# Kernel tuning notes

Measured on AMD Instinct MI355X. Metric: run time of the kernel, lower is better.

## Reference

```python
import jax, jax.numpy as jnp
import numpy as np

HIDDEN = 2048
REDUCTION = 4
DOWN = HIDDEN // REDUCTION  # 512
E = 16
K = 2
B, S = 4, 2048


def setup_inputs() -> dict:
    key = jax.random.key(0)
    k1, k2, k3, k4 = jax.random.split(key, 4)
    x = jax.random.normal(k1, (B, S, HIDDEN), dtype=jnp.float32)
    gate_w = jax.random.normal(k2, (E, HIDDEN), dtype=jnp.float32) * 0.02
    # xavier_uniform over (E, DOWN, HIDDEN): bound = sqrt(6/(DOWN+HIDDEN))
    bound = float(np.sqrt(6.0 / (DOWN + HIDDEN)))
    down_w = jax.random.uniform(k3, (E, DOWN, HIDDEN), dtype=jnp.float32,
                                minval=-bound, maxval=bound)
    down_b = jnp.zeros((E, DOWN), dtype=jnp.float32)
    ub = float(np.sqrt(1.0 / DOWN))
    up_w = jax.random.uniform(k4, (HIDDEN, DOWN), dtype=jnp.float32,
                              minval=-ub, maxval=ub)
    up_b = jnp.zeros((HIDDEN,), dtype=jnp.float32)
    return {"x": x, "gate_w": gate_w, "down_w": down_w, "down_b": down_b,
            "up_w": up_w, "up_b": up_b}


def reference(x, gate_w, down_w, down_b, up_w, up_b):
    Bb, Ss, D = x.shape
    N = Bb * Ss
    xf = x.reshape(N, D)
    # TopKGate: logits -> top-k -> softmax over the k logits -> scatter to full [N,E]
    logits = xf @ gate_w.T                       # [N, E]
    topv, topi = jax.lax.top_k(logits, K)        # [N, K]
    probs = jax.nn.softmax(topv, axis=-1)        # [N, K]
    gw = jnp.zeros_like(logits).at[jnp.arange(N)[:, None], topi].set(probs)  # [N, E]
    # Dense-equivalent of gather + per-token bmm + scatter-add combine:
    # final[n] = sum_e gw[n,e] * (down_w[e] @ x[n] + down_b[e])
    expert_out = jnp.einsum('nd,eod->neo', xf, down_w) + down_b[None]  # [N, E, DOWN]
    combined = jnp.einsum('ne,neo->no', gw, expert_out)                # [N, DOWN]
    h = jax.nn.gelu(combined, approximate=True)  # gelu_new (tanh approx)
    h = h.reshape(Bb, Ss, DOWN)
    out = h @ up_w.T + up_b                      # [B, S, HIDDEN]
    # load balancing loss: E * sum(sum(gw,0)/N * mean(gw,0)) * alpha
    loss = E * jnp.sum(jnp.sum(gw, axis=0) / N * jnp.mean(gw, axis=0)) * 0.1
    return out, loss
```

## Files before the change

kernel.cpp:

```cpp
#include <hip/hip_runtime.h>
#include <hip/hip_bf16.h>
#include <math.h>

#define NTOK   8192
#define HID    2048
#define DWN    512
#define NEXP   16
#define PADSLOT 18432

#define OFF_COMBINED 0
#define OFF_XB       16777216
#define OFF_DWB      50331648
#define OFF_UWB      83886080
#define OFF_H        85983232
#define OFF_TOK      94371840
#define OFF_PROB     94445568
#define OFF_EIDX     94519296
#define OFF_PVAL     94584832
#define OFF_COUNTS   94650368
#define OFF_BASE     94650432
#define OFF_CURSOR   94650560
#define OFF_COLSUM   94650624
#define WS_NEEDED    94650688

typedef __attribute__((ext_vector_type(8))) __bf16 bf16x8;
typedef __attribute__((ext_vector_type(4))) float f32x4;

#define ASYNC16(gsrc, ldst) \
  __builtin_amdgcn_global_load_lds((const __attribute__((address_space(1))) unsigned int*)(gsrc), \
                                   (__attribute__((address_space(3))) unsigned int*)(ldst), 16, 0, 0)

__device__ inline unsigned short f2bf(float f) {
  unsigned int u = __float_as_uint(f);
  unsigned int r = (u + 0x7FFFu + ((u >> 16) & 1u)) >> 16;
  return (unsigned short)r;
}

__global__ __launch_bounds__(256) void cast8_kernel(const float* __restrict__ src,
                                                    unsigned short* __restrict__ dst)
{
  size_t i = ((size_t)blockIdx.x * 256 + threadIdx.x) * 8;
  float4 a = *(const float4*)(src + i);
  float4 b = *(const float4*)(src + i + 4);
  unsigned short o[8];
  o[0]=f2bf(a.x); o[1]=f2bf(a.y); o[2]=f2bf(a.z); o[3]=f2bf(a.w);
  o[4]=f2bf(b.x); o[5]=f2bf(b.y); o[6]=f2bf(b.z); o[7]=f2bf(b.w);
  *(uint4*)(dst + i) = *(const uint4*)o;
}

__global__ __launch_bounds__(256) void gate_kernel(
    const float* __restrict__ x, const float* __restrict__ gw,
    int2* __restrict__ eidx, float2* __restrict__ pvals)
{
  int lane = threadIdx.x & 63;
  int wave = threadIdx.x >> 6;
  int n = blockIdx.x * 4 + wave;
  const float* xr  = x + (size_t)n * HID;
  const float* gwp = gw + lane;

  double a0=0,a1=0,a2=0,a3=0,a4=0,a5=0,a6=0,a7=0;
  double a8=0,a9=0,a10=0,a11=0,a12=0,a13=0,a14=0,a15=0;

  for (int d0 = 0; d0 < HID; d0 += 64) {
    double xd = (double)xr[d0 + lane];
    const float* g = gwp + d0;
    a0  = fma(xd, (double)g[ 0*HID], a0);
    a1  = fma(xd, (double)g[ 1*HID], a1);
    a2  = fma(xd, (double)g[ 2*HID], a2);
    a3  = fma(xd, (double)g[ 3*HID], a3);
    a4  = fma(xd, (double)g[ 4*HID], a4);
    a5  = fma(xd, (double)g[ 5*HID], a5);
    a6  = fma(xd, (double)g[ 6*HID], a6);
    a7  = fma(xd, (double)g[ 7*HID], a7);
    a8  = fma(xd, (double)g[ 8*HID], a8);
    a9  = fma(xd, (double)g[ 9*HID], a9);
    a10 = fma(xd, (double)g[10*HID], a10);
    a11 = fma(xd, (double)g[11*HID], a11);
    a12 = fma(xd, (double)g[12*HID], a12);
    a13 = fma(xd, (double)g[13*HID], a13);
    a14 = fma(xd, (double)g[14*HID], a14);
    a15 = fma(xd, (double)g[15*HID], a15);
  }

#define RED(v) { v += __shfl_xor(v,32,64); v += __shfl_xor(v,16,64); v += __shfl_xor(v,8,64); \
                 v += __shfl_xor(v,4,64);  v += __shfl_xor(v,2,64);  v += __shfl_xor(v,1,64); }
  RED(a0) RED(a1) RED(a2) RED(a3) RED(a4) RED(a5) RED(a6) RED(a7)
  RED(a8) RED(a9) RED(a10) RED(a11) RED(a12) RED(a13) RED(a14) RED(a15)
#undef RED

  if (lane == 0) {
    double v0 = -1e300, v1 = -1e300;
    int i0 = 0, i1 = 0;
#define TOP(v,E) { if ((v) > v0) { v1 = v0; i1 = i0; v0 = (v); i0 = (E); } \
                   else if ((v) > v1) { v1 = (v); i1 = (E); } }
    TOP(a0,0) TOP(a1,1) TOP(a2,2) TOP(a3,3) TOP(a4,4) TOP(a5,5) TOP(a6,6) TOP(a7,7)
    TOP(a8,8) TOP(a9,9) TOP(a10,10) TOP(a11,11) TOP(a12,12) TOP(a13,13) TOP(a14,14) TOP(a15,15)
#undef TOP
    double ex = exp(v1 - v0);
    double denom = 1.0 + ex;
    eidx[n]  = make_int2(i0, i1);
    pvals[n] = make_float2((float)(1.0 / denom), (float)(ex / denom));
  }
}

__global__ __launch_bounds__(256) void hist_kernel(
    const int2* __restrict__ eidx, const float2* __restrict__ pvals,
    int* __restrict__ counts, float* __restrict__ colsum)
{
  __shared__ int   cbin[NEXP];
  __shared__ float lbin[NEXP];
  if (threadIdx.x < NEXP) { cbin[threadIdx.x] = 0; lbin[threadIdx.x] = 0.f; }
  __syncthreads();
  int n = blockIdx.x * 256 + threadIdx.x;
  int2 e = eidx[n];
  float2 p = pvals[n];
  atomicAdd(&cbin[e.x], 1);  atomicAdd(&lbin[e.x], p.x);
  atomicAdd(&cbin[e.y], 1);  atomicAdd(&lbin[e.y], p.y);
  __syncthreads();
  if (threadIdx.x < NEXP) {
    atomicAdd(&counts[threadIdx.x], cbin[threadIdx.x]);
    atomicAdd(&colsum[threadIdx.x], lbin[threadIdx.x]);
  }
}

__global__ void scan_loss_kernel(const int* __restrict__ counts, int* __restrict__ base,
                                 const float* __restrict__ colsum, float* __restrict__ loss_out)
{
  if (threadIdx.x == 0 && blockIdx.x == 0) {
    int acc = 0;
    for (int e = 0; e < NEXP; e++) { base[e] = acc; acc += (counts[e] + 127) & ~127; }
    base[NEXP] = acc;
    double s = 0.0;
    for (int e = 0; e < NEXP; e++) { double c = (double)colsum[e]; s += c * c; }
    loss_out[0] = (float)(1.6 * s / ((double)NTOK * (double)NTOK));
  }
}

__global__ __launch_bounds__(256) void scatter_kernel(
    const int2* __restrict__ eidx, const float2* __restrict__ pvals,
    const int* __restrict__ base, int* __restrict__ cursor,
    int* __restrict__ tok, float* __restrict__ prob)
{
  int n = blockIdx.x * 256 + threadIdx.x;
  int lane = threadIdx.x & 63;
  int2 e = eidx[n];
  float2 p = pvals[n];
  int   myE[2] = {e.x, e.y};
  float myP[2] = {p.x, p.y};
#pragma unroll
  for (int s = 0; s < 2; s++) {
    int eq = myE[s];
#pragma unroll
    for (int q = 0; q < NEXP; q++) {
      unsigned long long m = __ballot(eq == q);
      if (eq == q) {
        int cnt = __popcll(m);
        int pre = __popcll(m & ((1ull << lane) - 1ull));
        int b = 0;
        if (pre == 0) b = atomicAdd(&cursor[q], cnt);
        int leader = __ffsll((long long)m) - 1;
        b = __shfl(b, leader, 64);
        int pos = base[q] + b + pre;
        tok[pos] = n; prob[pos] = myP[s];
      }
    }
  }
}

__global__ __launch_bounds__(256) void down_mfma_kernel(
    const unsigned short* __restrict__ xb, const unsigned short* __restrict__ dwb,
    const float* __restrict__ db,
    const int* __restrict__ base, const int* __restrict__ tok, const float* __restrict__ prob,
    float* __restrict__ combined)
{
  __shared__ unsigned short As[128 * 64];
  __shared__ unsigned short Bs[128 * 64];
  __shared__ int   tks[128];
  __shared__ float prs[128];

  int slot0 = blockIdx.x * 128;
  if (slot0 >= base[NEXP]) return;
  int e = 0;
#pragma unroll
  for (int q = 1; q < NEXP; q++) if (base[q] <= slot0) e = q;
  int out0 = blockIdx.y * 128;

  int tid = threadIdx.x;
  if (tid < 128) { tks[tid] = tok[slot0 + tid]; prs[tid] = prob[slot0 + tid]; }

  const int l = tid & 63, w = tid >> 6;
  const int wm = w & 1, wn = w >> 1;
  const int lm = l & 15, quad = l >> 4;

  const unsigned short* agp[4];
  const unsigned short* bgp[4];
#pragma unroll
  for (int i = 0; i < 4; i++) {
    int c = (w * 4 + i) * 64 + l;
    int r = c >> 3, kc = c & 7;
    int t = tok[slot0 + r];
    agp[i] = xb + (size_t)(t < 0 ? 0 : t) * HID + kc * 8;
    bgp[i] = dwb + ((size_t)e * DWN + out0 + r) * HID + kc * 8;
  }

  f32x4 acc[4][4] = {};

  for (int k0 = 0; k0 < HID; k0 += 64) {
    __syncthreads();
#pragma unroll
    for (int i = 0; i < 4; i++) {
      ASYNC16(agp[i] + k0, &As[(w * 4 + i) * 64 * 8]);
      ASYNC16(bgp[i] + k0, &Bs[(w * 4 + i) * 64 * 8]);
    }
    __syncthreads();
#pragma unroll
    for (int kk = 0; kk < 64; kk += 32) {
      bf16x8 af[4], bfr[4];
#pragma unroll
      for (int mi = 0; mi < 4; mi++)
        af[mi] = *(const bf16x8*)&As[(wm * 64 + mi * 16 + lm) * 64 + kk + quad * 8];
#pragma unroll
      for (int ni = 0; ni < 4; ni++)
        bfr[ni] = *(const bf16x8*)&Bs[(wn * 64 + ni * 16 + lm) * 64 + kk + quad * 8];
#pragma unroll
      for (int mi = 0; mi < 4; mi++)
#pragma unroll
        for (int ni = 0; ni < 4; ni++)
          acc[mi][ni] = __builtin_amdgcn_mfma_f32_16x16x32_bf16(af[mi], bfr[ni], acc[mi][ni], 0, 0, 0);
    }
  }

  float dbv[4];
#pragma unroll
  for (int ni = 0; ni < 4; ni++)
    dbv[ni] = db[e * DWN + out0 + wn * 64 + ni * 16 + lm];
#pragma unroll
  for (int mi = 0; mi < 4; mi++) {
#pragma unroll
    for (int reg = 0; reg < 4; reg++) {
      int m = wm * 64 + mi * 16 + quad * 4 + reg;
      int t = tks[m];
      if (t < 0) continue;
      float p = prs[m];
      float* crow = combined + (size_t)t * DWN;
#pragma unroll
      for (int ni = 0; ni < 4; ni++) {
        int gc = out0 + wn * 64 + ni * 16 + lm;
        atomicAdd(&crow[gc], p * (acc[mi][ni][reg] + dbv[ni]));
      }
    }
  }
}

__global__ __launch_bounds__(256) void gelu_cast_kernel(const float* __restrict__ c,
                                                        unsigned short* __restrict__ h)
{
  size_t i = ((size_t)blockIdx.x * 256 + threadIdx.x) * 8;
  float4 a = *(const float4*)(c + i);
  float4 b = *(const float4*)(c + i + 4);
  float f[8] = {a.x, a.y, a.z, a.w, b.x, b.y, b.z, b.w};
  unsigned short o[8];
#pragma unroll
  for (int j = 0; j < 8; j++) {
    float xx = f[j];
    float inner = 0.7978845608028654f * (xx + 0.044715f * xx * xx * xx);
    o[j] = f2bf(0.5f * xx * (1.0f + tanhf(inner)));
  }
  *(uint4*)(h + i) = *(const uint4*)o;
}

__global__ __launch_bounds__(256) void up_mfma_kernel(
    const unsigned short* __restrict__ h, const unsigned short* __restrict__ uwb,
    const float* __restrict__ ub, float* __restrict__ out)
{
  __shared__ unsigned short As[128 * 64];
  __shared__ unsigned short Bs[128 * 64];

  int row0 = blockIdx.x * 128;
  int col0 = blockIdx.y * 128;
  int tid = threadIdx.x;
  const int l = tid & 63, w = tid >> 6;
  const int wm = w & 1, wn = w >> 1;
  const int lm = l & 15, quad = l >> 4;

  const unsigned short* agp[4];
  const unsigned short* bgp[4];
#pragma unroll
  for (int i = 0; i < 4; i++) {
    int c = (w * 4 + i) * 64 + l;
    int r = c >> 3, kc = c & 7;
    agp[i] = h   + (size_t)(row0 + r) * DWN + kc * 8;
    bgp[i] = uwb + (size_t)(col0 + r) * DWN + kc * 8;
  }

  f32x4 acc[4][4] = {};

  for (int k0 = 0; k0 < DWN; k0 += 64) {
    __syncthreads();
#pragma unroll
    for (int i = 0; i < 4; i++) {
      ASYNC16(agp[i] + k0, &As[(w * 4 + i) * 64 * 8]);
      ASYNC16(bgp[i] + k0, &Bs[(w * 4 + i) * 64 * 8]);
    }
    __syncthreads();
#pragma unroll
    for (int kk = 0; kk < 64; kk += 32) {
      bf16x8 af[4], bfr[4];
#pragma unroll
      for (int mi = 0; mi < 4; mi++)
        af[mi] = *(const bf16x8*)&As[(wm * 64 + mi * 16 + lm) * 64 + kk + quad * 8];
#pragma unroll
      for (int ni = 0; ni < 4; ni++)
        bfr[ni] = *(const bf16x8*)&Bs[(wn * 64 + ni * 16 + lm) * 64 + kk + quad * 8];
#pragma unroll
      for (int mi = 0; mi < 4; mi++)
#pragma unroll
        for (int ni = 0; ni < 4; ni++)
          acc[mi][ni] = __builtin_amdgcn_mfma_f32_16x16x32_bf16(af[mi], bfr[ni], acc[mi][ni], 0, 0, 0);
    }
  }

  float ubv[4];
#pragma unroll
  for (int ni = 0; ni < 4; ni++)
    ubv[ni] = ub[col0 + wn * 64 + ni * 16 + lm];
#pragma unroll
  for (int mi = 0; mi < 4; mi++) {
#pragma unroll
    for (int reg = 0; reg < 4; reg++) {
      int m = row0 + wm * 64 + mi * 16 + quad * 4 + reg;
      float* orow = out + (size_t)m * HID;
#pragma unroll
      for (int ni = 0; ni < 4; ni++) {
        int gc = col0 + wn * 64 + ni * 16 + lm;
        orow[gc] = acc[mi][ni][reg] + ubv[ni];
      }
    }
  }
}

extern "C" void kernel_launch(void* const* d_in, const int* in_sizes, int n_in,
                              void* d_out, int out_size, void* d_ws, size_t ws_size,
                              hipStream_t stream)
{
  const float* x  = (const float*)d_in[0];
  const float* gw = (const float*)d_in[1];
  const float* dw = (const float*)d_in[2];
  const float* db = (const float*)d_in[3];
  const float* uw = (const float*)d_in[4];
  const float* ub = (const float*)d_in[5];
  float* out = (float*)d_out;

  char* ws = (char*)d_ws;
  float*          combined = (float*)(ws + OFF_COMBINED);
  unsigned short* xb       = (unsigned short*)(ws + OFF_XB);
  unsigned short* dwb      = (unsigned short*)(ws + OFF_DWB);
  unsigned short* uwb      = (unsigned short*)(ws + OFF_UWB);
  unsigned short* h        = (unsigned short*)(ws + OFF_H);
  int*    tok    = (int*)(ws + OFF_TOK);
  float*  prob   = (float*)(ws + OFF_PROB);
  int2*   eidx   = (int2*)(ws + OFF_EIDX);
  float2* pvals  = (float2*)(ws + OFF_PVAL);
  int*    counts = (int*)(ws + OFF_COUNTS);
  int*    base   = (int*)(ws + OFF_BASE);
  int*    cursor = (int*)(ws + OFF_CURSOR);
  float*  colsum = (float*)(ws + OFF_COLSUM);

  hipMemsetAsync(combined, 0, (size_t)NTOK * DWN * sizeof(float), stream);
  hipMemsetAsync(tok, 0xFF, PADSLOT * sizeof(int), stream);
  hipMemsetAsync(counts, 0, WS_NEEDED - OFF_COUNTS, stream);

  cast8_kernel<<<(NTOK * HID) / 8 / 256, 256, 0, stream>>>(x, xb);
  cast8_kernel<<<(NEXP * DWN * HID) / 8 / 256, 256, 0, stream>>>(dw, dwb);
  cast8_kernel<<<(HID * DWN) / 8 / 256, 256, 0, stream>>>(uw, uwb);

  gate_kernel<<<NTOK / 4, 256, 0, stream>>>(x, gw, eidx, pvals);
  hist_kernel<<<NTOK / 256, 256, 0, stream>>>(eidx, pvals, counts, colsum);
  scan_loss_kernel<<<1, 64, 0, stream>>>(counts, base, colsum, out + (size_t)NTOK * HID);
  scatter_kernel<<<NTOK / 256, 256, 0, stream>>>(eidx, pvals, base, cursor, tok, prob);

  dim3 gdown(PADSLOT / 128, DWN / 128);
  down_mfma_kernel<<<gdown, 256, 0, stream>>>(xb, dwb, db, base, tok, prob, combined);

  gelu_cast_kernel<<<(NTOK * DWN) / 8 / 256, 256, 0, stream>>>(combined, h);

  dim3 gup(NTOK / 128, HID / 128);
  up_mfma_kernel<<<gup, 256, 0, stream>>>(h, uwb, ub, out);
}
```

Baseline: 434.4 us.

## Replace atomic scatter-add combine with bf16 slot buffers and fused combine+GELU

```diff
diff --git a/kernel.cpp b/kernel.cpp
--- a/kernel.cpp
+++ b/kernel.cpp
@@ -8,20 +8,23 @@
 #define NEXP   16
 #define PADSLOT 18432
 
-#define OFF_COMBINED 0
-#define OFF_XB       16777216
-#define OFF_DWB      50331648
-#define OFF_UWB      83886080
-#define OFF_H        85983232
-#define OFF_TOK      94371840
-#define OFF_PROB     94445568
-#define OFF_EIDX     94519296
-#define OFF_PVAL     94584832
-#define OFF_COUNTS   94650368
-#define OFF_BASE     94650432
-#define OFF_CURSOR   94650560
-#define OFF_COLSUM   94650624
-#define WS_NEEDED    94650688
+#define OFF_XB       0
+#define OFF_DWB      33554432
+#define OFF_H        33554432
+#define OFF_UWB      67108864
+#define OFF_TOK      69206016
+#define OFF_SPOS     69279744
+#define OFF_EIDX     69345280
+#define OFF_PVAL     69410816
+#define OFF_COUNTS   69476352
+#define OFF_BASE     69476416
+#define OFF_CURSOR   69476544
+#define OFF_COLSUM   69476608
+#define OFF_SEG      69476672
+#define SEGHALF_SHORTS 9437184
+#define SEGHALF_BYTES  18874368
+#define WS_NEED1     (OFF_SEG + 1 * SEGHALF_BYTES)
+#define WS_NEED2     (OFF_SEG + 2 * SEGHALF_BYTES)
 
 typedef __attribute__((ext_vector_type(8))) __bf16 bf16x8;
 typedef __attribute__((ext_vector_type(4))) float f32x4;
@@ -34,6 +37,9 @@
   unsigned int u = __float_as_uint(f);
   unsigned int r = (u + 0x7FFFu + ((u >> 16) & 1u)) >> 16;
   return (unsigned short)r;
+}
+__device__ inline float bf2f(unsigned short s) {
+  return __uint_as_float((unsigned int)s << 16);
 }
 
 __global__ __launch_bounds__(256) void cast8_kernel(const float* __restrict__ src,
@@ -137,16 +143,14 @@
 }
 
 __global__ __launch_bounds__(256) void scatter_kernel(
-    const int2* __restrict__ eidx, const float2* __restrict__ pvals,
-    const int* __restrict__ base, int* __restrict__ cursor,
-    int* __restrict__ tok, float* __restrict__ prob)
+    const int2* __restrict__ eidx, const int* __restrict__ base, int* __restrict__ cursor,
+    int* __restrict__ tok, int2* __restrict__ spos)
 {
   int n = blockIdx.x * 256 + threadIdx.x;
   int lane = threadIdx.x & 63;
   int2 e = eidx[n];
-  float2 p = pvals[n];
-  int   myE[2] = {e.x, e.y};
-  float myP[2] = {p.x, p.y};
+  int myE[2] = {e.x, e.y};
+  int myPos[2];
 #pragma unroll
   for (int s = 0; s < 2; s++) {
     int eq = myE[s];
@@ -161,22 +165,22 @@
         int leader = __ffsll((long long)m) - 1;
         b = __shfl(b, leader, 64);
         int pos = base[q] + b + pre;
-        tok[pos] = n; prob[pos] = myP[s];
+        tok[pos] = n;
+        myPos[s] = pos;
       }
     }
   }
+  spos[n] = make_int2(myPos[0], myPos[1]);
 }
 
 __global__ __launch_bounds__(256) void down_mfma_kernel(
     const unsigned short* __restrict__ xb, const unsigned short* __restrict__ dwb,
-    const float* __restrict__ db,
-    const int* __restrict__ base, const int* __restrict__ tok, const float* __restrict__ prob,
-    float* __restrict__ combined)
-{
-  __shared__ unsigned short As[128 * 64];
-  __shared__ unsigned short Bs[128 * 64];
-  __shared__ int   tks[128];
-  __shared__ float prs[128];
+    const int* __restrict__ base, const int* __restrict__ tok,
+    unsigned short* __restrict__ seg, int kcount)
+{
+  __shared__ unsigned short smem[17408];
+  unsigned short* As = smem;
+  unsigned short* Bs = smem + 8192;
 
   int slot0 = blockIdx.x * 128;
   if (slot0 >= base[NEXP]) return;
@@ -184,10 +188,10 @@
 #pragma unroll
   for (int q = 1; q < NEXP; q++) if (base[q] <= slot0) e = q;
   int out0 = blockIdx.y * 128;
+  int kh   = blockIdx.z;
+  int kbase = kh * kcount * 64;
 
   int tid = threadIdx.x;
-  if (tid < 128) { tks[tid] = tok[slot0 + tid]; prs[tid] = prob[slot0 + tid]; }
-
   const int l = tid & 63, w = tid >> 6;
   const int wm = w & 1, wn = w >> 1;
   const int lm = l & 15, quad = l >> 4;
@@ -196,32 +200,42 @@
   const unsigned short* bgp[4];
 #pragma unroll
   for (int i = 0; i < 4; i++) {
-    int c = (w * 4 + i) * 64 + l;
-    int r = c >> 3, kc = c & 7;
+    int g = w * 4 + i;
+    int r = g * 8 + (l & 7);
+    int kc = l >> 3;
     int t = tok[slot0 + r];
-    agp[i] = xb + (size_t)(t < 0 ? 0 : t) * HID + kc * 8;
-    bgp[i] = dwb + ((size_t)e * DWN + out0 + r) * HID + kc * 8;
+    agp[i] = xb + (size_t)(t < 0 ? 0 : t) * HID + kbase + kc * 8;
+    bgp[i] = dwb + ((size_t)e * DWN + out0 + r) * HID + kbase + kc * 8;
+  }
+
+  int am_off[4], bn_off[4];
+#pragma unroll
+  for (int mi = 0; mi < 4; mi++) {
+    int m = wm * 64 + mi * 16 + lm;
+    am_off[mi] = (m >> 3) * 512 + (m & 7) * 8 + quad * 64;
+    int nn = wn * 64 + mi * 16 + lm;
+    bn_off[mi] = (nn >> 3) * 512 + (nn & 7) * 8 + quad * 64;
   }
 
   f32x4 acc[4][4] = {};
 
-  for (int k0 = 0; k0 < HID; k0 += 64) {
+  for (int it = 0; it < kcount; it++) {
+    int k0 = it * 64;
     __syncthreads();
 #pragma unroll
     for (int i = 0; i < 4; i++) {
-      ASYNC16(agp[i] + k0, &As[(w * 4 + i) * 64 * 8]);
-      ASYNC16(bgp[i] + k0, &Bs[(w * 4 + i) * 64 * 8]);
+      int g = w * 4 + i;
+      ASYNC16(agp[i] + k0, &As[g * 512]);
+      ASYNC16(bgp[i] + k0, &Bs[g * 512]);
     }
     __syncthreads();
 #pragma unroll
-    for (int kk = 0; kk < 64; kk += 32) {
+    for (int kk = 0; kk < 2; kk++) {
       bf16x8 af[4], bfr[4];
 #pragma unroll
-      for (int mi = 0; mi < 4; mi++)
-        af[mi] = *(const bf16x8*)&As[(wm * 64 + mi * 16 + lm) * 64 + kk + quad * 8];
-#pragma unroll
-      for (int ni = 0; ni < 4; ni++)
-        bfr[ni] = *(const bf16x8*)&Bs[(wn * 64 + ni * 16 + lm) * 64 + kk + quad * 8];
+      for (int mi = 0; mi < 4; mi++) af[mi]  = *(const bf16x8*)&As[am_off[mi] + kk * 256];
+#pragma unroll
+      for (int ni = 0; ni < 4; ni++) bfr[ni] = *(const bf16x8*)&Bs[bn_off[ni] + kk * 256];
 #pragma unroll
       for (int mi = 0; mi < 4; mi++)
 #pragma unroll
@@ -230,51 +244,72 @@
     }
   }
 
-  float dbv[4];
-#pragma unroll
-  for (int ni = 0; ni < 4; ni++)
-    dbv[ni] = db[e * DWN + out0 + wn * 64 + ni * 16 + lm];
-#pragma unroll
-  for (int mi = 0; mi < 4; mi++) {
+  __syncthreads();
+#pragma unroll
+  for (int mi = 0; mi < 4; mi++)
 #pragma unroll
     for (int reg = 0; reg < 4; reg++) {
       int m = wm * 64 + mi * 16 + quad * 4 + reg;
-      int t = tks[m];
-      if (t < 0) continue;
-      float p = prs[m];
-      float* crow = combined + (size_t)t * DWN;
 #pragma unroll
       for (int ni = 0; ni < 4; ni++) {
-        int gc = out0 + wn * 64 + ni * 16 + lm;
-        atomicAdd(&crow[gc], p * (acc[mi][ni][reg] + dbv[ni]));
+        int c = wn * 64 + ni * 16 + lm;
+        smem[m * 136 + c] = f2bf(acc[mi][ni][reg]);
       }
     }
-  }
-}
-
-__global__ __launch_bounds__(256) void gelu_cast_kernel(const float* __restrict__ c,
-                                                        unsigned short* __restrict__ h)
-{
-  size_t i = ((size_t)blockIdx.x * 256 + threadIdx.x) * 8;
-  float4 a = *(const float4*)(c + i);
-  float4 b = *(const float4*)(c + i + 4);
-  float f[8] = {a.x, a.y, a.z, a.w, b.x, b.y, b.z, b.w};
+  __syncthreads();
+#pragma unroll
+  for (int it2 = 0; it2 < 8; it2++) {
+    int chunk = it2 * 256 + tid;
+    int row = chunk >> 4, off = (chunk & 15) * 8;
+    uint4 v = *(const uint4*)&smem[row * 136 + off];
+    *(uint4*)&seg[(size_t)kh * SEGHALF_SHORTS + (size_t)(slot0 + row) * 512 + out0 + off] = v;
+  }
+}
+
+__global__ __launch_bounds__(256) void combine_gelu_kernel(
+    const unsigned short* __restrict__ seg, const int2* __restrict__ spos,
+    const float2* __restrict__ pv, const int2* __restrict__ eix,
+    const float* __restrict__ db, unsigned short* __restrict__ h, int ksplit)
+{
+  int n = blockIdx.x * 4 + (threadIdx.x >> 6);
+  int lane = threadIdx.x & 63;
+  int c0 = lane * 8;
+  int2 sp = spos[n];
+  float2 p = pv[n];
+  int2 e = eix[n];
+
+  float d0[8] = {0,0,0,0,0,0,0,0}, d1[8] = {0,0,0,0,0,0,0,0};
+  for (int hh = 0; hh < ksplit; hh++) {
+    uint4 u0 = *(const uint4*)(seg + (size_t)hh * SEGHALF_SHORTS + (size_t)sp.x * 512 + c0);
+    uint4 u1 = *(const uint4*)(seg + (size_t)hh * SEGHALF_SHORTS + (size_t)sp.y * 512 + c0);
+    const unsigned short* s0 = (const unsigned short*)&u0;
+    const unsigned short* s1 = (const unsigned short*)&u1;
+#pragma unroll
+    for (int j = 0; j < 8; j++) { d0[j] += bf2f(s0[j]); d1[j] += bf2f(s1[j]); }
+  }
+  float b0[8], b1[8];
+  *(float4*)&b0[0] = *(const float4*)(db + e.x * DWN + c0);
+  *(float4*)&b0[4] = *(const float4*)(db + e.x * DWN + c0 + 4);
+  *(float4*)&b1[0] = *(const float4*)(db + e.y * DWN + c0);
+  *(float4*)&b1[4] = *(const float4*)(db + e.y * DWN + c0 + 4);
+
   unsigned short o[8];
 #pragma unroll
   for (int j = 0; j < 8; j++) {
-    float xx = f[j];
+    float xx = p.x * (d0[j] + b0[j]) + p.y * (d1[j] + b1[j]);
     float inner = 0.7978845608028654f * (xx + 0.044715f * xx * xx * xx);
     o[j] = f2bf(0.5f * xx * (1.0f + tanhf(inner)));
   }
-  *(uint4*)(h + i) = *(const uint4*)o;
+  *(uint4*)(h + (size_t)n * DWN + c0) = *(const uint4*)o;
 }
 
 __global__ __launch_bounds__(256) void up_mfma_kernel(
     const unsigned short* __restrict__ h, const unsigned short* __restrict__ uwb,
     const float* __restrict__ ub, float* __restrict__ out)
 {
-  __shared__ unsigned short As[128 * 64];
-  __shared__ unsigned short Bs[128 * 64];
+  __shared__ unsigned short smem[16384];
+  unsigned short* As = smem;
+  unsigned short* Bs = smem + 8192;
 
   int row0 = blockIdx.x * 128;
   int col0 = blockIdx.y * 128;
@@ -287,31 +322,40 @@
   const unsigned short* bgp[4];
 #pragma unroll
   for (int i = 0; i < 4; i++) {
-    int c = (w * 4 + i) * 64 + l;
-    int r = c >> 3, kc = c & 7;
+    int g = w * 4 + i;
+    int r = g * 8 + (l & 7);
+    int kc = l >> 3;
     agp[i] = h   + (size_t)(row0 + r) * DWN + kc * 8;
     bgp[i] = uwb + (size_t)(col0 + r) * DWN + kc * 8;
   }
 
+  int am_off[4], bn_off[4];
+#pragma unroll
+  for (int mi = 0; mi < 4; mi++) {
+    int m = wm * 64 + mi * 16 + lm;
+    am_off[mi] = (m >> 3) * 512 + (m & 7) * 8 + quad * 64;
+    int nn = wn * 64 + mi * 16 + lm;
+    bn_off[mi] = (nn >> 3) * 512 + (nn & 7) * 8 + quad * 64;
+  }
+
   f32x4 acc[4][4] = {};
 
   for (int k0 = 0; k0 < DWN; k0 += 64) {
     __syncthreads();
 #pragma unroll
     for (int i = 0; i < 4; i++) {
-      ASYNC16(agp[i] + k0, &As[(w * 4 + i) * 64 * 8]);
-      ASYNC16(bgp[i] + k0, &Bs[(w * 4 + i) * 64 * 8]);
+      int g = w * 4 + i;
+      ASYNC16(agp[i] + k0, &As[g * 512]);
+      ASYNC16(bgp[i] + k0, &Bs[g * 512]);
     }
     __syncthreads();
 #pragma unroll
-    for (int kk = 0; kk < 64; kk += 32) {
+    for (int kk = 0; kk < 2; kk++) {
       bf16x8 af[4], bfr[4];
 #pragma unroll
-      for (int mi = 0; mi < 4; mi++)
-        af[mi] = *(const bf16x8*)&As[(wm * 64 + mi * 16 + lm) * 64 + kk + quad * 8];
-#pragma unroll
-      for (int ni = 0; ni < 4; ni++)
-        bfr[ni] = *(const bf16x8*)&Bs[(wn * 64 + ni * 16 + lm) * 64 + kk + quad * 8];
+      for (int mi = 0; mi < 4; mi++) af[mi]  = *(const bf16x8*)&As[am_off[mi] + kk * 256];
+#pragma unroll
+      for (int ni = 0; ni < 4; ni++) bfr[ni] = *(const bf16x8*)&Bs[bn_off[ni] + kk * 256];
 #pragma unroll
       for (int mi = 0; mi < 4; mi++)
 #pragma unroll
@@ -352,13 +396,13 @@
   float* out = (float*)d_out;
 
   char* ws = (char*)d_ws;
-  float*          combined = (float*)(ws + OFF_COMBINED);
-  unsigned short* xb       = (unsigned short*)(ws + OFF_XB);
-  unsigned short* dwb      = (unsigned short*)(ws + OFF_DWB);
-  unsigned short* uwb      = (unsigned short*)(ws + OFF_UWB);
-  unsigned short* h        = (unsigned short*)(ws + OFF_H);
+  unsigned short* xb   = (unsigned short*)(ws + OFF_XB);
+  unsigned short* dwb  = (unsigned short*)(ws + OFF_DWB);
+  unsigned short* uwb  = (unsigned short*)(ws + OFF_UWB);
+  unsigned short* h    = (unsigned short*)(ws + OFF_H);
+  unsigned short* seg  = (unsigned short*)(ws + OFF_SEG);
   int*    tok    = (int*)(ws + OFF_TOK);
-  float*  prob   = (float*)(ws + OFF_PROB);
+  int2*   spos   = (int2*)(ws + OFF_SPOS);
   int2*   eidx   = (int2*)(ws + OFF_EIDX);
   float2* pvals  = (float2*)(ws + OFF_PVAL);
   int*    counts = (int*)(ws + OFF_COUNTS);
@@ -366,9 +410,11 @@
   int*    cursor = (int*)(ws + OFF_CURSOR);
   float*  colsum = (float*)(ws + OFF_COLSUM);
 
-  hipMemsetAsync(combined, 0, (size_t)NTOK * DWN * sizeof(float), stream);
+  const int ksplit = (ws_size >= (size_t)WS_NEED2) ? 2 : 1;
+  const int kcount = (HID / 64) / ksplit;
+
   hipMemsetAsync(tok, 0xFF, PADSLOT * sizeof(int), stream);
-  hipMemsetAsync(counts, 0, WS_NEEDED - OFF_COUNTS, stream);
+  hipMemsetAsync(counts, 0, 320, stream);
 
   cast8_kernel<<<(NTOK * HID) / 8 / 256, 256, 0, stream>>>(x, xb);
   cast8_kernel<<<(NEXP * DWN * HID) / 8 / 256, 256, 0, stream>>>(dw, dwb);
@@ -377,12 +423,12 @@
   gate_kernel<<<NTOK / 4, 256, 0, stream>>>(x, gw, eidx, pvals);
   hist_kernel<<<NTOK / 256, 256, 0, stream>>>(eidx, pvals, counts, colsum);
   scan_loss_kernel<<<1, 64, 0, stream>>>(counts, base, colsum, out + (size_t)NTOK * HID);
-  scatter_kernel<<<NTOK / 256, 256, 0, stream>>>(eidx, pvals, base, cursor, tok, prob);
-
-  dim3 gdown(PADSLOT / 128, DWN / 128);
-  down_mfma_kernel<<<gdown, 256, 0, stream>>>(xb, dwb, db, base, tok, prob, combined);
-
-  gelu_cast_kernel<<<(NTOK * DWN) / 8 / 256, 256, 0, stream>>>(combined, h);
+  scatter_kernel<<<NTOK / 256, 256, 0, stream>>>(eidx, base, cursor, tok, spos);
+
+  dim3 gdown(PADSLOT / 128, DWN / 128, ksplit);
+  down_mfma_kernel<<<gdown, 256, 0, stream>>>(xb, dwb, base, tok, seg, kcount);
+
+  combine_gelu_kernel<<<NTOK / 4, 256, 0, stream>>>(seg, spos, pvals, eidx, db, h, ksplit);
 
   dim3 gup(NTOK / 128, HID / 128);
   up_mfma_kernel<<<gup, 256, 0, stream>>>(h, uwb, ub, out);
```

Measured after the change: 426.6 us. About the same (-1.8%).
